# Optimization experiments

Measured on AMD Instinct MI355X. Metric: run time of the kernel, lower is better.

Reference implementation:

```python
import jax, jax.numpy as jnp
import numpy as np

N_EXPERT_CAPACITY = 2  # init kwarg; k = S * capacity // E


def setup_inputs() -> dict:
    key = jax.random.key(0)
    k1, k2, k3, k4 = jax.random.split(key, 4)
    B, S, D, E, F = 8, 1024, 1024, 8, 2048
    # kaiming-uniform-ish scales
    x = jax.random.normal(k1, (B, S, D), dtype=jnp.float32)
    choice_w = jax.random.uniform(k2, (E, D), dtype=jnp.float32, minval=-1.0, maxval=1.0) * (1.0 / np.sqrt(D))
    w1 = jax.random.uniform(k3, (E, D, F), dtype=jnp.float32, minval=-1.0, maxval=1.0) * (1.0 / np.sqrt(D))
    w2 = jax.random.uniform(k4, (E, F, D), dtype=jnp.float32, minval=-1.0, maxval=1.0) * (1.0 / np.sqrt(F))
    return {"x": x, "choice_w": choice_w, "w1": w1, "w2": w2}


def reference(x, choice_w, w1, w2):
    B, S, D = x.shape
    E = choice_w.shape[0]
    k = S * N_EXPERT_CAPACITY // E  # tokens per expert (expert-choice)
    # router softmax over experts: [B, S, E]
    probs = jax.nn.softmax(jnp.einsum('bsd,ed->bse', x, choice_w), axis=-1)
    # each expert picks its top-k tokens: G, I are [B, E, k]
    G, I = jax.lax.top_k(jnp.swapaxes(probs, -1, -2), k)
    # dispatch: gather tokens instead of one-hot matmul (same math)
    x_in = jnp.take_along_axis(x[:, None, :, :], I[..., None], axis=2)  # [B, E, k, D]
    # per-expert MLP with SiLU
    h = jax.nn.silu(jnp.einsum('bekd,edf->bekf', x_in, w1))  # [B, E, k, F]
    x_mlp = jnp.einsum('bekf,efd->bekd', h, w2)              # [B, E, k, D]
    # combine: weighted scatter-add back to token positions (equals P,G,x_mlp einsum)
    b_idx = jnp.arange(B)[:, None, None]  # [B,1,1] broadcasts with I [B,E,k]
    out = jnp.zeros_like(x).at[b_idx, I].add(G[..., None] * x_mlp)
    return out
```

## Files before the change

### kernel.cpp

```cpp
#include <hip/hip_runtime.h>
#include <hip/hip_bf16.h>
#include <math.h>

#define B_   8
#define S_   1024
#define D_   1024
#define E_   8
#define F_   2048
#define KCAP 256

typedef __bf16 bf16x8 __attribute__((ext_vector_type(8)));
typedef float  floatx4 __attribute__((ext_vector_type(4)));
typedef unsigned short ushortx8 __attribute__((ext_vector_type(8)));

__device__ __forceinline__ unsigned short f2b(float f) {
    union { float f; unsigned int u; } v; v.f = f;
    unsigned int u = v.u;
    u += 0x7fffu + ((u >> 16) & 1u);
    return (unsigned short)(u >> 16);
}
__device__ __forceinline__ float b2f(unsigned short u) {
    union { unsigned int u; float f; } v; v.u = ((unsigned)u) << 16; return v.f;
}

__device__ __forceinline__ void gl_lds16(const void* g, void* l) {
    __builtin_amdgcn_global_load_lds(
        (const __attribute__((address_space(1))) void*)g,
        (__attribute__((address_space(3))) void*)l, 16, 0, 0);
}

__device__ __forceinline__ unsigned long long topk_key(float p, int s) {
    return (((unsigned long long)__float_as_uint(p)) << 10) | (unsigned)(S_ - 1 - s);
}

__global__ void router_kernel(const float* __restrict__ x, const float* __restrict__ cw,
                              float* __restrict__ probs, unsigned short* __restrict__ xb) {
    int gid  = blockIdx.x * 256 + threadIdx.x;
    int wave = gid >> 6;
    int lane = gid & 63;
    int b = wave >> 10;
    int s = wave & (S_ - 1);
    const float* xrow = x + ((size_t)b * S_ + s) * D_;
    unsigned short* xbrow = xb + ((size_t)b * S_ + s) * D_;
    float acc[E_];
#pragma unroll
    for (int e = 0; e < E_; e++) acc[e] = 0.f;
#pragma unroll
    for (int it = 0; it < D_ / 256; it++) {
        int i = it * 256 + lane * 4;
        float4 xv = *(const float4*)(xrow + i);
        ushort4 o;
        o.x = f2b(xv.x); o.y = f2b(xv.y); o.z = f2b(xv.z); o.w = f2b(xv.w);
        *(ushort4*)(xbrow + i) = o;
#pragma unroll
        for (int e = 0; e < E_; e++) {
            float4 wv = *(const float4*)(cw + e * D_ + i);
            acc[e] = fmaf(xv.x, wv.x, fmaf(xv.y, wv.y, fmaf(xv.z, wv.z, fmaf(xv.w, wv.w, acc[e]))));
        }
    }
#pragma unroll
    for (int e = 0; e < E_; e++) {
        float v = acc[e];
#pragma unroll
        for (int off = 32; off >= 1; off >>= 1) v += __shfl_down(v, off, 64);
        acc[e] = v;
    }
    if (lane == 0) {
        float m = acc[0];
#pragma unroll
        for (int e = 1; e < E_; e++) m = fmaxf(m, acc[e]);
        float sum = 0.f;
#pragma unroll
        for (int e = 0; e < E_; e++) { acc[e] = __expf(acc[e] - m); sum += acc[e]; }
        float inv = 1.f / sum;
#pragma unroll
        for (int e = 0; e < E_; e++) probs[((size_t)b * E_ + e) * S_ + s] = acc[e] * inv;
    }
}

__global__ void topk_kernel(const float* __restrict__ probs, int* __restrict__ I,
                            float* __restrict__ G, unsigned short* __restrict__ Pmap) {
    const int be = blockIdx.x;
    const int b = be >> 3, e = be & 7;
    const int tid = threadIdx.x;
    __shared__ unsigned long long keys[S_];
    const float* rowp = probs + (size_t)be * S_;
#pragma unroll
    for (int q = 0; q < 4; q++) {
        const int s = q * 256 + tid;
        keys[s] = topk_key(rowp[s], s);
        Pmap[((size_t)(b * S_ + s)) * E_ + e] = 0;
    }
    __syncthreads();
    unsigned long long my[4];
    int r[4] = {0, 0, 0, 0};
#pragma unroll
    for (int q = 0; q < 4; q++) my[q] = keys[q * 256 + tid];
#pragma unroll 8
    for (int t = 0; t < S_; t++) {
        const unsigned long long kt = keys[t];
#pragma unroll
        for (int q = 0; q < 4; q++) r[q] += (kt > my[q]);
    }
#pragma unroll
    for (int q = 0; q < 4; q++) {
        if (r[q] < KCAP) {
            const int s = q * 256 + tid;
            I[be * KCAP + r[q]] = s;
            G[be * KCAP + r[q]] = rowp[s];
            Pmap[((size_t)(b * S_ + s)) * E_ + e] = (unsigned short)(r[q] + 1);
        }
    }
}

__global__ void transpose_cvt_kernel(const float* __restrict__ in, unsigned short* __restrict__ out,
                                     int R, int C) {
    __shared__ float tile[32][33];
    int e = blockIdx.z;
    int c0 = blockIdx.x * 32, r0 = blockIdx.y * 32;
    const float* ine = in + (size_t)e * R * C;
    unsigned short* oute = out + (size_t)e * R * C;
    int tid = threadIdx.x;
    int row = tid >> 3, cs = tid & 7;
    float4 v = *(const float4*)(ine + (size_t)(r0 + row) * C + c0 + cs * 4);
    tile[row][cs * 4 + 0] = v.x; tile[row][cs * 4 + 1] = v.y;
    tile[row][cs * 4 + 2] = v.z; tile[row][cs * 4 + 3] = v.w;
    __syncthreads();
    int c = tid >> 3, rq = tid & 7;
    ushort4 o;
    o.x = f2b(tile[rq * 4 + 0][c]); o.y = f2b(tile[rq * 4 + 1][c]);
    o.z = f2b(tile[rq * 4 + 2][c]); o.w = f2b(tile[rq * 4 + 3][c]);
    *(ushort4*)(oute + (size_t)(c0 + c) * R + r0 + rq * 4) = o;
}


#define GBAR() __builtin_amdgcn_s_barrier()

#define LDA4(I0, BUF) do { \
    _Pragma("unroll") \
    for (int ii = 0; ii < 4; ii++) { \
        const int o_ = (BUF) * 16384 + aRd + ((I0) + ii) * 1024; \
        aF[(I0) + ii][0] = *(const bf16x8*)&Asm[o_]; \
        aF[(I0) + ii][1] = *(const bf16x8*)&Asm[o_ ^ 32]; \
    } } while (0)

#define LDB2(J0, BUF) do { \
    _Pragma("unroll") \
    for (int jj = 0; jj < 2; jj++) { \
        const int o_ = (BUF) * 16384 + bRd + ((J0) + jj) * 1024; \
        bF[(J0) + jj][0] = *(const bf16x8*)&Bsm[o_]; \
        bF[(J0) + jj][1] = *(const bf16x8*)&Bsm[o_ ^ 32]; \
    } } while (0)

#define MMQ(I0, J0) do { \
    __builtin_amdgcn_s_setprio(1); \
    _Pragma("unroll") \
    for (int ii = 0; ii < 4; ii++) \
    _Pragma("unroll") \
    for (int jj = 0; jj < 2; jj++) { \
        acc[(I0)+ii][(J0)+jj] = __builtin_amdgcn_mfma_f32_16x16x32_bf16(aF[(I0)+ii][0], bF[(J0)+jj][0], acc[(I0)+ii][(J0)+jj], 0, 0, 0); \
        acc[(I0)+ii][(J0)+jj] = __builtin_amdgcn_mfma_f32_16x16x32_bf16(aF[(I0)+ii][1], bF[(J0)+jj][1], acc[(I0)+ii][(J0)+jj], 0, 0, 0); \
    } \
    __builtin_amdgcn_s_setprio(0); \
} while (0)

#define STAGE_A(T, HH) do { if ((T) < NKT) { \
    const unsigned k_ = (unsigned)(T) * 64u; \
    const int d_ = ((((T) & 1) * 2 + (HH)) * 8192) + dst0; \
    gl_lds16(gA + srcA[(HH) * 2 + 0] + k_, &Asm[d_]); \
    gl_lds16(gA + srcA[(HH) * 2 + 1] + k_, &Asm[d_ + 4096]); \
} } while (0)

#define STAGE_B(T, HH) do { if ((T) < NKT) { \
    const unsigned k_ = (unsigned)(T) * 64u; \
    const int d_ = ((((T) & 1) * 2 + (HH)) * 8192) + dst0; \
    gl_lds16(gB + srcB[(HH) * 2 + 0] + k_, &Bsm[d_]); \
    gl_lds16(gB + srcB[(HH) * 2 + 1] + k_, &Bsm[d_ + 4096]); \
} } while (0)

#define PROLOGUE() do { \
    STAGE_A(0, 0); STAGE_A(0, 1); STAGE_B(0, 0); STAGE_B(0, 1); \
    STAGE_A(1, 0); STAGE_B(1, 0); \
    asm volatile("s_waitcnt vmcnt(4)" ::: "memory"); \
    GBAR(); \
} while (0)

#define KLOOP() \
    _Pragma("unroll 1") \
    for (int t = 0; t < NKT; t += 2) { \
        LDA4(0, 0); LDB2(0, 0); STAGE_A(t + 1, 1); \
        GBAR(); MMQ(0, 0); GBAR(); \
        LDA4(4, 0); LDB2(2, 0); STAGE_B(t + 1, 1); \
        GBAR(); MMQ(4, 2); GBAR(); \
        STAGE_A(t + 2, 0); \
        GBAR(); MMQ(0, 2); GBAR(); \
        STAGE_B(t + 2, 0); \
        if (t + 2 < NKT) { asm volatile("s_waitcnt vmcnt(4)" ::: "memory"); } \
        else             { asm volatile("s_waitcnt vmcnt(0)" ::: "memory"); } \
        GBAR(); MMQ(4, 0); GBAR(); \
        LDA4(0, 1); LDB2(0, 1); STAGE_A(t + 2, 1); \
        GBAR(); MMQ(0, 0); GBAR(); \
        LDA4(4, 1); LDB2(2, 1); STAGE_B(t + 2, 1); \
        GBAR(); MMQ(4, 2); GBAR(); \
        STAGE_A(t + 3, 0); \
        GBAR(); MMQ(0, 2); GBAR(); \
        STAGE_B(t + 3, 0); \
        asm volatile("s_waitcnt vmcnt(4)" ::: "memory"); \
        GBAR(); MMQ(4, 0); GBAR(); \
    }

__global__ __launch_bounds__(512, 2) void gemm1_kernel(
    const unsigned short* __restrict__ xb,
    const unsigned short* __restrict__ w1t,
    const int* __restrict__ Ibuf,
    unsigned short* __restrict__ H)
{
    const int g  = blockIdx.x;
    const int e  = g & 7;
    const int rr = g >> 3;
    const int b  = rr >> 3;
    const int nt = rr & 7;
    const int be = b * 8 + e;
    const int tid = threadIdx.x;
    constexpr int NKT = D_ / 64;

    __shared__ __align__(16) unsigned short Asm[2 * 2 * 128 * 64];
    __shared__ __align__(16) unsigned short Bsm[2 * 2 * 128 * 64];

    const int r0   = tid >> 3;
    const int kseg = (tid & 7) ^ (r0 & 7);
    const int dst0 = tid * 8;

    const unsigned short* gA = xb;
    const unsigned short* gB = w1t;
    unsigned srcA[4], srcB[4];
#pragma unroll
    for (int q = 0; q < 4; q++) {
        const int m = q * 64 + r0;
        const int tok = Ibuf[be * KCAP + m];
        srcA[q] = (unsigned)((b * S_ + tok) * D_ + kseg * 8);
        srcB[q] = (unsigned)((e * F_ + nt * 256 + m) * D_ + kseg * 8);
    }

    const int lane = tid & 63;
    const int wv   = tid >> 6;
    const int wm2  = wv >> 2;
    const int wn4  = wv & 3;
    const int l15  = lane & 15;
    const int quad = lane >> 4;
    const int x0   = (quad ^ (l15 & 7)) * 8;
    const int aRd  = wm2 * 8192 + l15 * 64 + x0;
    const int bRd  = (wn4 >> 1) * 8192 + ((wn4 & 1) * 64 + l15) * 64 + x0;

    floatx4 acc[8][4];
#pragma unroll
    for (int i = 0; i < 8; i++)
#pragma unroll
        for (int j = 0; j < 4; j++) acc[i][j] = (floatx4){0.f, 0.f, 0.f, 0.f};
    bf16x8 aF[8][2], bF[4][2];

    PROLOGUE();
    KLOOP();

    unsigned short* Hbe = H + (size_t)be * KCAP * F_ + (nt * 256 + wn4 * 64);
#pragma unroll
    for (int i = 0; i < 8; i++) {
#pragma unroll
        for (int r2 = 0; r2 < 4; r2++) {
            const int m = wm2 * 128 + i * 16 + quad * 4 + r2;
            unsigned short* hrow = Hbe + (size_t)m * F_;
#pragma unroll
            for (int j = 0; j < 4; j++) {
                const float v = acc[i][j][r2];
                hrow[j * 16 + l15] = f2b(v / (1.f + __expf(-v)));
            }
        }
    }
}

__global__ __launch_bounds__(512, 2) void gemm2_kernel(
    const unsigned short* __restrict__ H,
    const unsigned short* __restrict__ w2t,
    unsigned short* __restrict__ xmlp)
{
    const int g  = blockIdx.x;
    const int e  = g & 7;
    const int rr = g >> 3;
    const int b  = rr >> 2;
    const int nt = rr & 3;
    const int be = b * 8 + e;
    const int tid = threadIdx.x;
    constexpr int NKT = F_ / 64;

    __shared__ __align__(16) unsigned short Asm[2 * 2 * 128 * 64];
    __shared__ __align__(16) unsigned short Bsm[2 * 2 * 128 * 64];

    const int r0   = tid >> 3;
    const int kseg = (tid & 7) ^ (r0 & 7);
    const int dst0 = tid * 8;

    const unsigned short* gA = H;
    const unsigned short* gB = w2t;
    unsigned srcA[4], srcB[4];
#pragma unroll
    for (int q = 0; q < 4; q++) {
        const int m = q * 64 + r0;
        srcA[q] = (unsigned)((be * KCAP + m) * F_ + kseg * 8);
        srcB[q] = (unsigned)((e * D_ + nt * 256 + m) * F_ + kseg * 8);
    }

    const int lane = tid & 63;
    const int wv   = tid >> 6;
    const int wm2  = wv >> 2;
    const int wn4  = wv & 3;
    const int l15  = lane & 15;
    const int quad = lane >> 4;
    const int x0   = (quad ^ (l15 & 7)) * 8;
    const int aRd  = wm2 * 8192 + l15 * 64 + x0;
    const int bRd  = (wn4 >> 1) * 8192 + ((wn4 & 1) * 64 + l15) * 64 + x0;

    floatx4 acc[8][4];
#pragma unroll
    for (int i = 0; i < 8; i++)
#pragma unroll
        for (int j = 0; j < 4; j++) acc[i][j] = (floatx4){0.f, 0.f, 0.f, 0.f};
    bf16x8 aF[8][2], bF[4][2];

    PROLOGUE();
    KLOOP();

    unsigned short* Xbe = xmlp + (size_t)be * KCAP * D_ + (nt * 256 + wn4 * 64);
#pragma unroll
    for (int i = 0; i < 8; i++) {
#pragma unroll
        for (int r2 = 0; r2 < 4; r2++) {
            const int m = wm2 * 128 + i * 16 + quad * 4 + r2;
            unsigned short* orow = Xbe + (size_t)m * D_;
#pragma unroll
            for (int j = 0; j < 4; j++)
                orow[j * 16 + l15] = f2b(acc[i][j][r2]);
        }
    }
}

__global__ void combine_kernel(const unsigned short* __restrict__ xmlp,
                               const unsigned short* __restrict__ Pmap,
                               const float* __restrict__ G,
                               float* __restrict__ out) {
    int gid  = blockIdx.x * 256 + threadIdx.x;
    int wave = gid >> 6;
    int lane = gid & 63;
    int b = wave >> 10;
    float acc[16];
#pragma unroll
    for (int i = 0; i < 16; i++) acc[i] = 0.f;
    const unsigned short* pm = Pmap + (size_t)wave * E_;
#pragma unroll
    for (int e = 0; e < E_; e++) {
        int pe = pm[e];
        if (pe) {
            int beslot = (b * E_ + e) * KCAP + (pe - 1);
            float g = G[beslot];
            const unsigned short* rw = xmlp + (size_t)beslot * D_ + lane * 16;
            ushortx8 r0 = *(const ushortx8*)(rw);
            ushortx8 r1 = *(const ushortx8*)(rw + 8);
#pragma unroll
            for (int i = 0; i < 8; i++) {
                acc[i]     = fmaf(g, b2f(r0[i]), acc[i]);
                acc[8 + i] = fmaf(g, b2f(r1[i]), acc[8 + i]);
            }
        }
    }
    float* orow = out + (size_t)wave * D_ + lane * 16;
    ((float4*)orow)[0] = make_float4(acc[0],  acc[1],  acc[2],  acc[3]);
    ((float4*)orow)[1] = make_float4(acc[4],  acc[5],  acc[6],  acc[7]);
    ((float4*)orow)[2] = make_float4(acc[8],  acc[9],  acc[10], acc[11]);
    ((float4*)orow)[3] = make_float4(acc[12], acc[13], acc[14], acc[15]);
}

extern "C" void kernel_launch(void* const* d_in, const int* in_sizes, int n_in,
                              void* d_out, int out_size, void* d_ws, size_t ws_size,
                              hipStream_t stream) {
    const float* x  = (const float*)d_in[0];
    const float* cw = (const float*)d_in[1];
    const float* w1 = (const float*)d_in[2];
    const float* w2 = (const float*)d_in[3];
    float* out = (float*)d_out;

    char* ws = (char*)d_ws;
    float*          probs = (float*)(ws);
    int*            Ibuf  = (int*)(ws + 262144);
    float*          Gbuf  = (float*)(ws + 327680);
    unsigned short* Pmap  = (unsigned short*)(ws + 393216);
    unsigned short* xb    = (unsigned short*)(ws + 524288);
    unsigned short* wT    = (unsigned short*)(ws + 17301504);
    unsigned short* Hbuf  = (unsigned short*)(ws + 50855936);
    unsigned short* xmlp  = (unsigned short*)(ws + 117964800);

    router_kernel<<<(B_ * S_ * 64) / 256, 256, 0, stream>>>(x, cw, probs, xb);
    topk_kernel<<<B_ * E_, 256, 0, stream>>>(probs, Ibuf, Gbuf, Pmap);
    transpose_cvt_kernel<<<dim3(F_ / 32, D_ / 32, E_), 256, 0, stream>>>(w1, wT, D_, F_);
    gemm1_kernel<<<B_ * E_ * (F_ / 256), 512, 0, stream>>>(xb, wT, Ibuf, Hbuf);
    transpose_cvt_kernel<<<dim3(D_ / 32, F_ / 32, E_), 256, 0, stream>>>(w2, wT, F_, D_);
    gemm2_kernel<<<B_ * E_ * (D_ / 256), 512, 0, stream>>>(Hbuf, wT, xmlp);
    combine_kernel<<<(B_ * S_ * 64) / 256, 256, 0, stream>>>(xmlp, Pmap, Gbuf, out);
}
```

Measured before the change: 419.4 us.

## Reorder gemm1 pipeline with fewer A fragments; replace gemm2 with simple 128x128 tile kernel

gemm1 keeps its double-buffered pipeline but reorders the quadrant MMA sequence so only four A fragments stay live, and it wraps barriers in sched_barrier to pin instruction scheduling. gemm2 is replaced by a simpler 256-thread kernel with 128x128 tiles, single-buffered LDS, and __syncthreads around each K step, launched with four times as many blocks. The aim is lower register pressure and higher occupancy. The cost is that gemm2 loses load/compute overlap and its operand reuse per block drops.

```diff
diff --git a/kernel.cpp b/kernel.cpp
--- a/kernel.cpp
+++ b/kernel.cpp
@@ -134,17 +134,18 @@
 }
 
 
-#define GBAR() __builtin_amdgcn_s_barrier()
-
-#define LDA4(I0, BUF) do { \
+#define SB0()  __builtin_amdgcn_sched_barrier(0)
+#define BARX() do { SB0(); __builtin_amdgcn_s_barrier(); SB0(); } while (0)
+
+#define LDA_SET(SET, BUF) do { \
     _Pragma("unroll") \
     for (int ii = 0; ii < 4; ii++) { \
-        const int o_ = (BUF) * 16384 + aRd + ((I0) + ii) * 1024; \
-        aF[(I0) + ii][0] = *(const bf16x8*)&Asm[o_]; \
-        aF[(I0) + ii][1] = *(const bf16x8*)&Asm[o_ ^ 32]; \
+        const int o_ = (BUF) * 16384 + aRd + ((SET) + ii) * 1024; \
+        aF[ii][0] = *(const bf16x8*)&Asm[o_]; \
+        aF[ii][1] = *(const bf16x8*)&Asm[o_ ^ 32]; \
     } } while (0)
 
-#define LDB2(J0, BUF) do { \
+#define LDB_SET(J0, BUF) do { \
     _Pragma("unroll") \
     for (int jj = 0; jj < 2; jj++) { \
         const int o_ = (BUF) * 16384 + bRd + ((J0) + jj) * 1024; \
@@ -158,8 +159,8 @@
     for (int ii = 0; ii < 4; ii++) \
     _Pragma("unroll") \
     for (int jj = 0; jj < 2; jj++) { \
-        acc[(I0)+ii][(J0)+jj] = __builtin_amdgcn_mfma_f32_16x16x32_bf16(aF[(I0)+ii][0], bF[(J0)+jj][0], acc[(I0)+ii][(J0)+jj], 0, 0, 0); \
-        acc[(I0)+ii][(J0)+jj] = __builtin_amdgcn_mfma_f32_16x16x32_bf16(aF[(I0)+ii][1], bF[(J0)+jj][1], acc[(I0)+ii][(J0)+jj], 0, 0, 0); \
+        acc[(I0)+ii][(J0)+jj] = __builtin_amdgcn_mfma_f32_16x16x32_bf16(aF[ii][0], bF[(J0)+jj][0], acc[(I0)+ii][(J0)+jj], 0, 0, 0); \
+        acc[(I0)+ii][(J0)+jj] = __builtin_amdgcn_mfma_f32_16x16x32_bf16(aF[ii][1], bF[(J0)+jj][1], acc[(I0)+ii][(J0)+jj], 0, 0, 0); \
     } \
     __builtin_amdgcn_s_setprio(0); \
 } while (0)
@@ -177,37 +178,6 @@
     gl_lds16(gB + srcB[(HH) * 2 + 0] + k_, &Bsm[d_]); \
     gl_lds16(gB + srcB[(HH) * 2 + 1] + k_, &Bsm[d_ + 4096]); \
 } } while (0)
-
-#define PROLOGUE() do { \
-    STAGE_A(0, 0); STAGE_A(0, 1); STAGE_B(0, 0); STAGE_B(0, 1); \
-    STAGE_A(1, 0); STAGE_B(1, 0); \
-    asm volatile("s_waitcnt vmcnt(4)" ::: "memory"); \
-    GBAR(); \
-} while (0)
-
-#define KLOOP() \
-    _Pragma("unroll 1") \
-    for (int t = 0; t < NKT; t += 2) { \
-        LDA4(0, 0); LDB2(0, 0); STAGE_A(t + 1, 1); \
-        GBAR(); MMQ(0, 0); GBAR(); \
-        LDA4(4, 0); LDB2(2, 0); STAGE_B(t + 1, 1); \
-        GBAR(); MMQ(4, 2); GBAR(); \
-        STAGE_A(t + 2, 0); \
-        GBAR(); MMQ(0, 2); GBAR(); \
-        STAGE_B(t + 2, 0); \
-        if (t + 2 < NKT) { asm volatile("s_waitcnt vmcnt(4)" ::: "memory"); } \
-        else             { asm volatile("s_waitcnt vmcnt(0)" ::: "memory"); } \
-        GBAR(); MMQ(4, 0); GBAR(); \
-        LDA4(0, 1); LDB2(0, 1); STAGE_A(t + 2, 1); \
-        GBAR(); MMQ(0, 0); GBAR(); \
-        LDA4(4, 1); LDB2(2, 1); STAGE_B(t + 2, 1); \
-        GBAR(); MMQ(4, 2); GBAR(); \
-        STAGE_A(t + 3, 0); \
-        GBAR(); MMQ(0, 2); GBAR(); \
-        STAGE_B(t + 3, 0); \
-        asm volatile("s_waitcnt vmcnt(4)" ::: "memory"); \
-        GBAR(); MMQ(4, 0); GBAR(); \
-    }
 
 __global__ __launch_bounds__(512, 2) void gemm1_kernel(
     const unsigned short* __restrict__ xb,
@@ -257,10 +227,35 @@
     for (int i = 0; i < 8; i++)
 #pragma unroll
         for (int j = 0; j < 4; j++) acc[i][j] = (floatx4){0.f, 0.f, 0.f, 0.f};
-    bf16x8 aF[8][2], bF[4][2];
-
-    PROLOGUE();
-    KLOOP();
+    bf16x8 aF[4][2], bF[4][2];
+
+    STAGE_A(0, 0); STAGE_A(0, 1); STAGE_B(0, 0); STAGE_B(0, 1);
+    STAGE_B(1, 0); STAGE_A(1, 0);
+    asm volatile("s_waitcnt vmcnt(4)" ::: "memory");
+    BARX();
+
+#pragma unroll 1
+    for (int t = 0; t < NKT; t += 2) {
+        LDA_SET(0, 0); LDB_SET(0, 0); STAGE_A(t + 1, 1);
+        BARX(); MMQ(0, 0); BARX();
+        LDB_SET(2, 0); STAGE_B(t + 1, 1);
+        BARX(); MMQ(0, 2); BARX();
+        LDA_SET(4, 0); STAGE_B(t + 2, 0);
+        BARX(); MMQ(4, 2); BARX();
+        STAGE_A(t + 2, 0);
+        if (t + 2 < NKT) { asm volatile("s_waitcnt vmcnt(4)" ::: "memory"); }
+        else             { asm volatile("s_waitcnt vmcnt(0)" ::: "memory"); }
+        BARX(); MMQ(4, 0); BARX();
+        LDA_SET(0, 1); LDB_SET(0, 1); STAGE_A(t + 2, 1);
+        BARX(); MMQ(0, 0); BARX();
+        LDB_SET(2, 1); STAGE_B(t + 2, 1);
+        BARX(); MMQ(0, 2); BARX();
+        LDA_SET(4, 1); STAGE_B(t + 3, 0);
+        BARX(); MMQ(4, 2); BARX();
+        STAGE_A(t + 3, 0);
+        asm volatile("s_waitcnt vmcnt(4)" ::: "memory");
+        BARX(); MMQ(4, 0); BARX();
+    }
 
     unsigned short* Hbe = H + (size_t)be * KCAP * F_ + (nt * 256 + wn4 * 64);
 #pragma unroll
@@ -278,7 +273,7 @@
     }
 }
 
-__global__ __launch_bounds__(512, 2) void gemm2_kernel(
+__global__ __launch_bounds__(256, 4) void gemm2_kernel(
     const unsigned short* __restrict__ H,
     const unsigned short* __restrict__ w2t,
     unsigned short* __restrict__ xmlp)
@@ -286,59 +281,83 @@
     const int g  = blockIdx.x;
     const int e  = g & 7;
     const int rr = g >> 3;
-    const int b  = rr >> 2;
-    const int nt = rr & 3;
+    const int b  = rr >> 4;
+    const int t4 = rr & 15;
     const int be = b * 8 + e;
+    const int mt = t4 & 1;
+    const int nt = t4 >> 1;
     const int tid = threadIdx.x;
-    constexpr int NKT = F_ / 64;
-
-    __shared__ __align__(16) unsigned short Asm[2 * 2 * 128 * 64];
-    __shared__ __align__(16) unsigned short Bsm[2 * 2 * 128 * 64];
-
-    const int r0   = tid >> 3;
-    const int kseg = (tid & 7) ^ (r0 & 7);
-    const int dst0 = tid * 8;
-
-    const unsigned short* gA = H;
-    const unsigned short* gB = w2t;
-    unsigned srcA[4], srcB[4];
-#pragma unroll
-    for (int q = 0; q < 4; q++) {
-        const int m = q * 64 + r0;
-        srcA[q] = (unsigned)((be * KCAP + m) * F_ + kseg * 8);
-        srcB[q] = (unsigned)((e * D_ + nt * 256 + m) * F_ + kseg * 8);
-    }
+
+    __shared__ __align__(16) unsigned short Asm2[128 * 64];
+    __shared__ __align__(16) unsigned short Bsm2[128 * 64];
+
+    const int r8   = tid >> 3;
+    const int kseg = (tid & 7) ^ (r8 & 7);
+    const size_t aoff0 = ((size_t)be * KCAP + mt * 128 + r8) * F_ + kseg * 8;
+    const size_t boff0 = ((size_t)e * D_ + nt * 128 + r8) * F_ + kseg * 8;
 
     const int lane = tid & 63;
     const int wv   = tid >> 6;
-    const int wm2  = wv >> 2;
-    const int wn4  = wv & 3;
+    const int wm   = (wv & 1) * 64;
+    const int wn   = (wv >> 1) * 64;
     const int l15  = lane & 15;
     const int quad = lane >> 4;
     const int x0   = (quad ^ (l15 & 7)) * 8;
-    const int aRd  = wm2 * 8192 + l15 * 64 + x0;
-    const int bRd  = (wn4 >> 1) * 8192 + ((wn4 & 1) * 64 + l15) * 64 + x0;
-
-    floatx4 acc[8][4];
-#pragma unroll
-    for (int i = 0; i < 8; i++)
+
+    int aoffs[4], boffs[4];
+#pragma unroll
+    for (int i = 0; i < 4; i++) {
+        aoffs[i] = (wm + i * 16 + l15) * 64 + x0;
+        boffs[i] = (wn + i * 16 + l15) * 64 + x0;
+    }
+
+    floatx4 acc[4][4];
+#pragma unroll
+    for (int i = 0; i < 4; i++)
 #pragma unroll
         for (int j = 0; j < 4; j++) acc[i][j] = (floatx4){0.f, 0.f, 0.f, 0.f};
-    bf16x8 aF[8][2], bF[4][2];
-
-    PROLOGUE();
-    KLOOP();
-
-    unsigned short* Xbe = xmlp + (size_t)be * KCAP * D_ + (nt * 256 + wn4 * 64);
-#pragma unroll
-    for (int i = 0; i < 8; i++) {
-#pragma unroll
-        for (int r2 = 0; r2 < 4; r2++) {
-            const int m = wm2 * 128 + i * 16 + quad * 4 + r2;
-            unsigned short* orow = Xbe + (size_t)m * D_;
+
+    for (int k0 = 0; k0 < F_; k0 += 64) {
+#pragma unroll
+        for (int w = 0; w < 4; w++) {
+            gl_lds16(H   + aoff0 + (size_t)w * 32 * F_ + k0, &Asm2[(w * 256 + tid) * 8]);
+            gl_lds16(w2t + boff0 + (size_t)w * 32 * F_ + k0, &Bsm2[(w * 256 + tid) * 8]);
+        }
+        __syncthreads();
+        bf16x8 af[4], bfr[4];
+#pragma unroll
+        for (int i = 0; i < 4; i++) {
+            af[i]  = *(const bf16x8*)&Asm2[aoffs[i]];
+            bfr[i] = *(const bf16x8*)&Bsm2[boffs[i]];
+        }
+#pragma unroll
+        for (int i = 0; i < 4; i++)
 #pragma unroll
             for (int j = 0; j < 4; j++)
-                orow[j * 16 + l15] = f2b(acc[i][j][r2]);
+                acc[i][j] = __builtin_amdgcn_mfma_f32_16x16x32_bf16(af[i], bfr[j], acc[i][j], 0, 0, 0);
+#pragma unroll
+        for (int i = 0; i < 4; i++) {
+            af[i]  = *(const bf16x8*)&Asm2[aoffs[i] ^ 32];
+            bfr[i] = *(const bf16x8*)&Bsm2[boffs[i] ^ 32];
+        }
+#pragma unroll
+        for (int i = 0; i < 4; i++)
+#pragma unroll
+            for (int j = 0; j < 4; j++)
+                acc[i][j] = __builtin_amdgcn_mfma_f32_16x16x32_bf16(af[i], bfr[j], acc[i][j], 0, 0, 0);
+        __syncthreads();
+    }
+
+    unsigned short* Xbe = xmlp + (size_t)be * KCAP * D_;
+#pragma unroll
+    for (int i = 0; i < 4; i++) {
+#pragma unroll
+        for (int r = 0; r < 4; r++) {
+            int m = mt * 128 + wm + i * 16 + quad * 4 + r;
+            unsigned short* orow = Xbe + (size_t)m * D_ + nt * 128;
+#pragma unroll
+            for (int j = 0; j < 4; j++)
+                orow[wn + j * 16 + l15] = f2b(acc[i][j][r]);
         }
     }
 }
@@ -402,6 +421,6 @@
     transpose_cvt_kernel<<<dim3(F_ / 32, D_ / 32, E_), 256, 0, stream>>>(w1, wT, D_, F_);
     gemm1_kernel<<<B_ * E_ * (F_ / 256), 512, 0, stream>>>(xb, wT, Ibuf, Hbuf);
     transpose_cvt_kernel<<<dim3(D_ / 32, F_ / 32, E_), 256, 0, stream>>>(w2, wT, F_, D_);
-    gemm2_kernel<<<B_ * E_ * (D_ / 256), 512, 0, stream>>>(Hbuf, wT, xmlp);
+    gemm2_kernel<<<B_ * E_ * 2 * (D_ / 128), 256, 0, stream>>>(Hbuf, wT, xmlp);
     combine_kernel<<<(B_ * S_ * 64) / 256, 256, 0, stream>>>(xmlp, Pmap, Gbuf, out);
 }
```

Result: faster. 387.5 us (-7.6%).
